# Kernel tuning notes

Hardware: AMD Instinct MI355X
Metric: run time of the kernel (lower is better)

## Reference

```python
import jax, jax.numpy as jnp
import numpy as np

N = 100000  # nodes
E = 1600000  # edges
F = 128      # nfeat == nclass (source constructs every layer as nfeat->nclass)


def setup_inputs() -> dict:
    key = jax.random.key(0)
    ks = jax.random.split(key, 8)
    x = jax.random.normal(ks[0], (N, F), dtype=jnp.float32)
    row = jax.random.randint(ks[1], (E,), 0, N)
    col = jax.random.randint(ks[2], (E,), 0, N)
    s = (1.0 / np.sqrt(F)).astype(np.float32) if hasattr(1.0/np.sqrt(F), 'astype') else 1.0/np.sqrt(F)
    s = 1.0 / np.sqrt(F)
    W0 = jax.random.uniform(ks[3], (F, F), jnp.float32, -s, s)
    b0 = jax.random.uniform(ks[4], (F,), jnp.float32, -s, s)
    W1 = jax.random.uniform(ks[5], (F, F), jnp.float32, -s, s)
    b1 = jax.random.uniform(ks[6], (F,), jnp.float32, -s, s)
    return {"x": x, "W0": W0, "b0": b0, "W1": W1, "b1": b1, "row": row, "col": col}


def _gcn_layer(h_in, W, b, row, col, dinv):
    # h = Linear(feat)
    h = h_in @ W + b
    # (D^-1/2 (A+I) D^-1/2) @ h, A in COO (row=i, col=j), A[i,j]=1
    coef = dinv[row] * dinv[col]                      # [E]
    msg = h[col] * coef[:, None]                       # [E, F] gather
    agg = jax.ops.segment_sum(msg, row, num_segments=N)
    agg = agg + (dinv * dinv)[:, None] * h             # self loops (identity)
    return agg


def reference(x, W0, b0, W1, b1, row, col):
    # D_hat = diag((A + I).sum(0)) -> column sums + 1
    deg = jax.ops.segment_sum(jnp.ones((E,), jnp.float32), col, num_segments=N) + 1.0
    dinv = deg ** -0.5
    h = _gcn_layer(x, W0, b0, row, col, dinv)
    h = jax.nn.relu(h)            # with_relu=True; dropout off (eval mode)
    h = _gcn_layer(h, W1, b1, row, col, dinv)
    return jax.nn.log_softmax(h, axis=1)
```

## Files before the change

### kernel.cpp

```cpp
#include <hip/hip_runtime.h>
#include <math.h>

#define FDIM 128
#define RPB 256
#define BSTRIDE 32
#define NBLK 512
#define MAXB 512
#define NSUB 8
#define SCAP 1024
#define CAP (NSUB * SCAP)

typedef __attribute__((ext_vector_type(8))) short short8;
typedef __attribute__((ext_vector_type(4))) float floatx4;

static __device__ __forceinline__ unsigned short f2bf(float f) {
    unsigned int u = __float_as_uint(f);
    u = (u + 0x7fff + ((u >> 16) & 1)) >> 16;
    return (unsigned short)u;
}

static __device__ __forceinline__ unsigned int cvtpk(float a, float b) {
    unsigned int r;
    asm("v_cvt_pk_bf16_f32 %0, %1, %2" : "=v"(r) : "v"(a), "v"(b));
    return r;
}

static __device__ __forceinline__ void bf2f(unsigned int u, float& a, float& b) {
    a = __uint_as_float(u << 16);
    b = __uint_as_float(u & 0xffff0000u);
}


__global__ __launch_bounds__(256) void k_init(int* rbCnt, int* cbCnt, int nb, unsigned int* hsz,
                                              const float* __restrict__ W0, const float* __restrict__ W1,
                                              unsigned short* __restrict__ W0t, unsigned short* __restrict__ W1t) {
    const int b = blockIdx.x;
    const int tid = threadIdx.x;
    if (b >= 2) {
        int i0 = (b - 2) * 256 + tid;
        int tot = nb * NSUB;
        for (int i = i0; i < tot; i += (gridDim.x - 2) * 256) {
            rbCnt[(size_t)i * BSTRIDE] = 0;
            cbCnt[(size_t)i * BSTRIDE] = 0;
        }
        if (b == 2 && tid < 64) hsz[tid] = 0u;
    } else {
        const float* W = (b == 0) ? W0 : W1;
        unsigned short* Wt = (b == 0) ? W0t : W1t;
        for (int idx = tid; idx < FDIM * FDIM; idx += 256) {
            int k = idx >> 7, c = idx & 127;
            Wt[c * FDIM + k] = f2bf(W[idx]);
        }
    }
}


__global__ __launch_bounds__(256) void k_scatter(const int* __restrict__ row, const int* __restrict__ col,
                                                 int* rbCnt, int* cbCnt,
                                                 unsigned int* __restrict__ pairs,
                                                 unsigned char* __restrict__ clocal, int nE, int nb) {
    __shared__ int rh[MAXB];
    __shared__ int ch[MAXB];
    __shared__ int rbase[MAXB];
    __shared__ int cbase[MAXB];
    const int tid = threadIdx.x;
    const int sub = blockIdx.x & (NSUB - 1);
    const int cpb = (nE + NBLK - 1) / NBLK;
    const int e0 = blockIdx.x * cpb;
    int e1 = e0 + cpb; if (e1 > nE) e1 = nE;

    for (int i = tid; i < nb; i += 256) { rh[i] = 0; ch[i] = 0; }
    __syncthreads();
    for (int e = e0 + tid; e < e1; e += 256) {
        atomicAdd(&rh[row[e] >> 8], 1);
        atomicAdd(&ch[col[e] >> 8], 1);
    }
    __syncthreads();
    for (int i = tid; i < nb; i += 256) {
        rbase[i] = rh[i] ? (i * CAP + sub * SCAP +
                            atomicAdd(&rbCnt[(size_t)(i * NSUB + sub) * BSTRIDE], rh[i])) : 0;
        cbase[i] = ch[i] ? (i * CAP + sub * SCAP +
                            atomicAdd(&cbCnt[(size_t)(i * NSUB + sub) * BSTRIDE], ch[i])) : 0;
        rh[i] = 0;
        ch[i] = 0;
    }
    __syncthreads();
    const int pmax = nb * CAP - 1;
    for (int e = e0 + tid; e < e1; e += 256) {
        int r = row[e];
        int c = col[e];
        int rb = r >> 8, cb = c >> 8;
        int p = rbase[rb] + atomicAdd(&rh[rb], 1);
        if (p > pmax) p = pmax;
        pairs[p] = ((unsigned int)(r & (RPB - 1)) << 24) | (unsigned int)c;
        int q = cbase[cb] + atomicAdd(&ch[cb], 1);
        if (q > pmax) q = pmax;
        clocal[q] = (unsigned char)(c & (RPB - 1));
    }
}


__global__ __launch_bounds__(256) void k_sortdinv(const int* __restrict__ rbCnt, const int* __restrict__ cbCnt,
                                                  const unsigned int* __restrict__ pairs,
                                                  const unsigned char* __restrict__ clocal,
                                                  uint2* __restrict__ rse, float* __restrict__ dinv,
                                                  int* __restrict__ csr_col, int n, int nb) {
    __shared__ int chist[RPB];
    __shared__ int hist[RPB];
    __shared__ int scan[RPB];
    __shared__ int lcur[RPB];
    const int b = blockIdx.x;
    const int tid = threadIdx.x;
    const int row0 = b * RPB;

    hist[tid] = 0;
    chist[tid] = 0;
    __syncthreads();
#pragma unroll
    for (int s = 0; s < NSUB; s++) {
        int rc = rbCnt[(size_t)(b * NSUB + s) * BSTRIDE]; if (rc > SCAP) rc = SCAP;
        int cc = cbCnt[(size_t)(b * NSUB + s) * BSTRIDE]; if (cc > SCAP) cc = SCAP;
        const int seg0 = b * CAP + s * SCAP;
        for (int i = seg0 + tid; i < seg0 + rc; i += 256)
            atomicAdd(&hist[pairs[i] >> 24], 1);
        for (int i = seg0 + tid; i < seg0 + cc; i += 256)
            atomicAdd(&chist[(int)clocal[i]], 1);
    }
    __syncthreads();

    scan[tid] = hist[tid];
    __syncthreads();
    for (int off = 1; off < RPB; off <<= 1) {
        int t = (tid >= off) ? scan[tid - off] : 0;
        __syncthreads();
        scan[tid] += t;
        __syncthreads();
    }
    {
        int ex = b * CAP + scan[tid] - hist[tid];
        lcur[tid] = ex;
        int r = row0 + tid;
        if (r < n) {
            rse[r] = make_uint2((unsigned int)ex, (unsigned int)(ex + hist[tid]));
            dinv[r] = rsqrtf((float)chist[tid] + 1.0f);
        }
    }
    __syncthreads();

#pragma unroll
    for (int s = 0; s < NSUB; s++) {
        int rc = rbCnt[(size_t)(b * NSUB + s) * BSTRIDE]; if (rc > SCAP) rc = SCAP;
        const int seg0 = b * CAP + s * SCAP;
        for (int i = seg0 + tid; i < seg0 + rc; i += 256) {
            unsigned int u = pairs[i];
            int pos = atomicAdd(&lcur[u >> 24], 1);
            csr_col[pos] = (int)(u & 0x00FFFFFFu);
        }
    }
}


#define KH 64
#define LPAD 72

__global__ __launch_bounds__(256) void k_gemm_mfma(const void* __restrict__ Ain,
                                                   const unsigned short* __restrict__ Wt,
                                                   const float* __restrict__ bias,
                                                   const float* __restrict__ dinv,
                                                   unsigned int* __restrict__ outp, int n, int af32) {
    __shared__ unsigned short sA[128][LPAD];
    __shared__ unsigned short sW[128][LPAD];

    const unsigned short* A = (const unsigned short*)Ain;
    const float* Af = (const float*)Ain;

    const int tid = threadIdx.x;
    const int row0 = blockIdx.x * 128;
    const int wid = tid >> 6;
    const int lane = tid & 63;
    const int quad = lane >> 4;
    const int lq = lane & 15;
    const int wm = wid & 1;
    const int wn = wid >> 1;

    floatx4 acc[4][4];
#pragma unroll
    for (int i = 0; i < 4; i++)
#pragma unroll
        for (int j = 0; j < 4; j++) acc[i][j] = (floatx4){0.f, 0.f, 0.f, 0.f};

    for (int kh = 0; kh < 2; kh++) {
        if (kh) __syncthreads();
#pragma unroll
        for (int it = 0; it < 4; it++) {
            int f = tid + it * 256;
            int r = f >> 3;
            int c8 = (f & 7) * 8;
            int gr = row0 + r;
            if (af32) {
                float4 v0 = make_float4(0.f, 0.f, 0.f, 0.f);
                float4 v1 = make_float4(0.f, 0.f, 0.f, 0.f);
                if (gr < n) {
                    v0 = *(const float4*)&Af[(size_t)gr * FDIM + kh * KH + c8];
                    v1 = *(const float4*)&Af[(size_t)gr * FDIM + kh * KH + c8 + 4];
                }
                uint4 p;
                p.x = cvtpk(v0.x, v0.y);
                p.y = cvtpk(v0.z, v0.w);
                p.z = cvtpk(v1.x, v1.y);
                p.w = cvtpk(v1.z, v1.w);
                *(uint4*)&sA[r][c8] = p;
            } else {
                uint4 v = make_uint4(0u, 0u, 0u, 0u);
                if (gr < n) v = *(const uint4*)&A[(size_t)gr * FDIM + kh * KH + c8];
                *(uint4*)&sA[r][c8] = v;
            }
            uint4 wv = *(const uint4*)&Wt[(size_t)r * FDIM + kh * KH + c8];
            *(uint4*)&sW[r][c8] = wv;
        }
        __syncthreads();

#pragma unroll
        for (int kt = 0; kt < 2; kt++) {
            const int k0 = kt * 32 + quad * 8;
            short8 af[4], bf[4];
#pragma unroll
            for (int mt = 0; mt < 4; mt++)
                af[mt] = *(const short8*)&sA[wm * 64 + mt * 16 + lq][k0];
#pragma unroll
            for (int nt = 0; nt < 4; nt++)
                bf[nt] = *(const short8*)&sW[wn * 64 + nt * 16 + lq][k0];
#pragma unroll
            for (int mt = 0; mt < 4; mt++)
#pragma unroll
                for (int nt = 0; nt < 4; nt++)
                    acc[mt][nt] = __builtin_amdgcn_mfma_f32_16x16x32_bf16(af[mt], bf[nt], acc[mt][nt], 0, 0, 0);
        }
    }

    float bv[4];
#pragma unroll
    for (int nt = 0; nt < 4; nt++) bv[nt] = bias[wn * 64 + nt * 16 + lq];

#pragma unroll
    for (int mt = 0; mt < 4; mt++) {
#pragma unroll
        for (int r = 0; r < 4; r++) {
            int grow = row0 + wm * 64 + mt * 16 + quad * 4 + r;
            float di = (grow < n) ? dinv[grow] : 0.f;
#pragma unroll
            for (int nt = 0; nt < 4; nt++) {
                float v = (acc[mt][nt][r] + bv[nt]) * di;
                float pv = __shfl_xor(v, 1, 64);
                if (!(lq & 1) && grow < n) {
                    int col = wn * 64 + nt * 16 + lq;
                    outp[(size_t)grow * 64 + (col >> 1)] =
                        (unsigned int)f2bf(v) | ((unsigned int)f2bf(pv) << 16);
                }
            }
        }
    }
}


#define UACC(U) { float p_, q_; \
    bf2f(U.x, p_, q_); acc0 += p_; acc1 += q_; \
    bf2f(U.y, p_, q_); acc2 += p_; acc3 += q_; \
    bf2f(U.z, p_, q_); acc4 += p_; acc5 += q_; \
    bf2f(U.w, p_, q_); acc6 += p_; acc7 += q_; }

__global__ __launch_bounds__(256) void k_agg(const unsigned int* __restrict__ hs,
                                             const uint2* __restrict__ rse,
                                             const int* __restrict__ csr_col, const float* __restrict__ dinv,
                                             void* __restrict__ out, int n, int relu, int lsm, int obf) {
    int w = (blockIdx.x * 256 + threadIdx.x) >> 6;
    int lane = threadIdx.x & 63;
    if (w >= n) return;
    const int quad = lane >> 4;
    const int lq = lane & 15;

    const uint2 se = rse[w];
    int e = (int)se.x;
    const int end = (int)se.y;
    const float di = dinv[w];

    uint4 sv = make_uint4(0u, 0u, 0u, 0u);
    if (quad == 0) sv = *(const uint4*)&hs[(size_t)w * 64 + lq * 4];
    float acc0, acc1, acc2, acc3, acc4, acc5, acc6, acc7;
    bf2f(sv.x, acc0, acc1);
    bf2f(sv.y, acc2, acc3);
    bf2f(sv.z, acc4, acc5);
    bf2f(sv.w, acc6, acc7);

    const int zrow = n;

    while (e < end) {
        int cnt = end - e;
        if (cnt > 64) cnt = 64;
        int jv = (e + lane < end) ? csr_col[e + lane] : zrow;
        int nb8 = (cnt + 7) >> 3;
        for (int t = 0; t < nb8; t++) {
            int i0 = t * 8 + quad;
            int j0 = __shfl(jv, i0, 64);
            int j1 = __shfl(jv, i0 + 4, 64);
            uint4 u0 = *(const uint4*)&hs[(size_t)j0 * 64 + lq * 4];
            uint4 u1 = *(const uint4*)&hs[(size_t)j1 * 64 + lq * 4];
            UACC(u0)
            UACC(u1)
        }
        e += cnt;
    }

    acc0 += __shfl_xor(acc0, 16, 64); acc0 += __shfl_xor(acc0, 32, 64);
    acc1 += __shfl_xor(acc1, 16, 64); acc1 += __shfl_xor(acc1, 32, 64);
    acc2 += __shfl_xor(acc2, 16, 64); acc2 += __shfl_xor(acc2, 32, 64);
    acc3 += __shfl_xor(acc3, 16, 64); acc3 += __shfl_xor(acc3, 32, 64);
    acc4 += __shfl_xor(acc4, 16, 64); acc4 += __shfl_xor(acc4, 32, 64);
    acc5 += __shfl_xor(acc5, 16, 64); acc5 += __shfl_xor(acc5, 32, 64);
    acc6 += __shfl_xor(acc6, 16, 64); acc6 += __shfl_xor(acc6, 32, 64);
    acc7 += __shfl_xor(acc7, 16, 64); acc7 += __shfl_xor(acc7, 32, 64);

    acc0 *= di; acc1 *= di; acc2 *= di; acc3 *= di;
    acc4 *= di; acc5 *= di; acc6 *= di; acc7 *= di;
    if (relu) {
        acc0 = fmaxf(acc0, 0.f); acc1 = fmaxf(acc1, 0.f);
        acc2 = fmaxf(acc2, 0.f); acc3 = fmaxf(acc3, 0.f);
        acc4 = fmaxf(acc4, 0.f); acc5 = fmaxf(acc5, 0.f);
        acc6 = fmaxf(acc6, 0.f); acc7 = fmaxf(acc7, 0.f);
    }
    if (lsm) {
        float m = fmaxf(fmaxf(fmaxf(acc0, acc1), fmaxf(acc2, acc3)),
                        fmaxf(fmaxf(acc4, acc5), fmaxf(acc6, acc7)));
#pragma unroll
        for (int off = 1; off < 16; off <<= 1) m = fmaxf(m, __shfl_xor(m, off, 64));
        float s = ((expf(acc0 - m) + expf(acc1 - m)) + (expf(acc2 - m) + expf(acc3 - m))) +
                  ((expf(acc4 - m) + expf(acc5 - m)) + (expf(acc6 - m) + expf(acc7 - m)));
#pragma unroll
        for (int off = 1; off < 16; off <<= 1) s += __shfl_xor(s, off, 64);
        float lg = m + logf(s);
        acc0 -= lg; acc1 -= lg; acc2 -= lg; acc3 -= lg;
        acc4 -= lg; acc5 -= lg; acc6 -= lg; acc7 -= lg;
    }
    if (obf) {
        if (quad == 0) {
            uint4 o;
            o.x = (unsigned int)f2bf(acc0) | ((unsigned int)f2bf(acc1) << 16);
            o.y = (unsigned int)f2bf(acc2) | ((unsigned int)f2bf(acc3) << 16);
            o.z = (unsigned int)f2bf(acc4) | ((unsigned int)f2bf(acc5) << 16);
            o.w = (unsigned int)f2bf(acc6) | ((unsigned int)f2bf(acc7) << 16);
            *(uint4*)((unsigned int*)out + (size_t)w * 64 + lq * 4) = o;
        }
    } else {
        if (quad < 2) {
            float4 o = quad ? make_float4(acc4, acc5, acc6, acc7)
                            : make_float4(acc0, acc1, acc2, acc3);
            *(float4*)((float*)out + (size_t)w * 128 + lq * 8 + quad * 4) = o;
        }
    }
}


extern "C" void kernel_launch(void* const* d_in, const int* in_sizes, int n_in,
                              void* d_out, int out_size, void* d_ws, size_t ws_size,
                              hipStream_t stream) {
    const float* x  = (const float*)d_in[0];
    const float* W0 = (const float*)d_in[1];
    const float* b0 = (const float*)d_in[2];
    const float* W1 = (const float*)d_in[3];
    const float* b1 = (const float*)d_in[4];
    const int* row  = (const int*)d_in[5];
    const int* col  = (const int*)d_in[6];
    float* out = (float*)d_out;

    const int N = in_sizes[0] / FDIM;
    const int E = in_sizes[5];
    const int NB = (N + RPB - 1) / RPB;

    char* w = (char*)d_ws;
    size_t off = 0;
    auto alloc = [&](size_t bytes) {
        char* p = w + off;
        off += (bytes + 255) & ~(size_t)255;
        return p;
    };
    int* rbCnt   = (int*)alloc((size_t)NB * NSUB * BSTRIDE * 4);
    int* cbCnt   = (int*)alloc((size_t)NB * NSUB * BSTRIDE * 4);
    float* dinv  = (float*)alloc((size_t)N * 4);
    uint2* rse   = (uint2*)alloc((size_t)N * 8);
    int* csr_col = (int*)alloc((size_t)NB * CAP * 4);
    unsigned short* W0t = (unsigned short*)alloc((size_t)FDIM * FDIM * 2);
    unsigned short* W1t = (unsigned short*)alloc((size_t)FDIM * FDIM * 2);
    unsigned int* hs = (unsigned int*)alloc((size_t)(N + 1) * 64 * 4);
    size_t pairsSz = (size_t)NB * CAP * 4;
    size_t clocSz  = (size_t)NB * CAP;
    size_t uniSz   = pairsSz + clocSz + 512;
    size_t hbSz    = (size_t)N * 64 * 4;
    char* uni = (char*)alloc(uniSz > hbSz ? uniSz : hbSz);
    unsigned int* pairs = (unsigned int*)uni;
    unsigned char* clocal = (unsigned char*)(uni + pairsSz);
    unsigned int* hb = (unsigned int*)uni;

    const int gW = (N * 64 + 255) / 256;
    const int gG = (N + 127) / 128;

    k_init<<<18, 256, 0, stream>>>(rbCnt, cbCnt, NB, hs + (size_t)N * 64, W0, W1, W0t, W1t);
    k_scatter<<<NBLK, 256, 0, stream>>>(row, col, rbCnt, cbCnt, pairs, clocal, E, NB);
    k_sortdinv<<<NB, 256, 0, stream>>>(rbCnt, cbCnt, pairs, clocal, rse, dinv, csr_col, N, NB);

    k_gemm_mfma<<<gG, 256, 0, stream>>>((const void*)x, W0t, b0, dinv, hs, N, 1);
    k_agg<<<gW, 256, 0, stream>>>(hs, rse, csr_col, dinv, hb, N, 1, 0, 1);

    k_gemm_mfma<<<gG, 256, 0, stream>>>((const void*)hb, W1t, b1, dinv, hs, N, 0);
    k_agg<<<gW, 256, 0, stream>>>(hs, rse, csr_col, dinv, out, N, 0, 1, 0);
}
```

Measured before the change: 353.8 us.

## Fuse first-layer GEMM into scatter kernel and move dinv scaling into aggregation

```diff
diff --git a/kernel.cpp b/kernel.cpp
--- a/kernel.cpp
+++ b/kernel.cpp
@@ -32,6 +32,7 @@
 
 
 __global__ __launch_bounds__(256) void k_init(int* rbCnt, int* cbCnt, int nb, unsigned int* hsz,
+                                              float* dinvN,
                                               const float* __restrict__ W0, const float* __restrict__ W1,
                                               unsigned short* __restrict__ W0t, unsigned short* __restrict__ W1t) {
     const int b = blockIdx.x;
@@ -44,6 +45,7 @@
             cbCnt[(size_t)i * BSTRIDE] = 0;
         }
         if (b == 2 && tid < 64) hsz[tid] = 0u;
+        if (b == 2 && tid == 64) *dinvN = 0.0f;
     } else {
         const float* W = (b == 0) ? W0 : W1;
         unsigned short* Wt = (b == 0) ? W0t : W1t;
@@ -55,127 +57,24 @@
 }
 
 
-__global__ __launch_bounds__(256) void k_scatter(const int* __restrict__ row, const int* __restrict__ col,
-                                                 int* rbCnt, int* cbCnt,
-                                                 unsigned int* __restrict__ pairs,
-                                                 unsigned char* __restrict__ clocal, int nE, int nb) {
-    __shared__ int rh[MAXB];
-    __shared__ int ch[MAXB];
-    __shared__ int rbase[MAXB];
-    __shared__ int cbase[MAXB];
-    const int tid = threadIdx.x;
-    const int sub = blockIdx.x & (NSUB - 1);
-    const int cpb = (nE + NBLK - 1) / NBLK;
-    const int e0 = blockIdx.x * cpb;
-    int e1 = e0 + cpb; if (e1 > nE) e1 = nE;
-
-    for (int i = tid; i < nb; i += 256) { rh[i] = 0; ch[i] = 0; }
-    __syncthreads();
-    for (int e = e0 + tid; e < e1; e += 256) {
-        atomicAdd(&rh[row[e] >> 8], 1);
-        atomicAdd(&ch[col[e] >> 8], 1);
-    }
-    __syncthreads();
-    for (int i = tid; i < nb; i += 256) {
-        rbase[i] = rh[i] ? (i * CAP + sub * SCAP +
-                            atomicAdd(&rbCnt[(size_t)(i * NSUB + sub) * BSTRIDE], rh[i])) : 0;
-        cbase[i] = ch[i] ? (i * CAP + sub * SCAP +
-                            atomicAdd(&cbCnt[(size_t)(i * NSUB + sub) * BSTRIDE], ch[i])) : 0;
-        rh[i] = 0;
-        ch[i] = 0;
-    }
-    __syncthreads();
-    const int pmax = nb * CAP - 1;
-    for (int e = e0 + tid; e < e1; e += 256) {
-        int r = row[e];
-        int c = col[e];
-        int rb = r >> 8, cb = c >> 8;
-        int p = rbase[rb] + atomicAdd(&rh[rb], 1);
-        if (p > pmax) p = pmax;
-        pairs[p] = ((unsigned int)(r & (RPB - 1)) << 24) | (unsigned int)c;
-        int q = cbase[cb] + atomicAdd(&ch[cb], 1);
-        if (q > pmax) q = pmax;
-        clocal[q] = (unsigned char)(c & (RPB - 1));
-    }
-}
-
-
-__global__ __launch_bounds__(256) void k_sortdinv(const int* __restrict__ rbCnt, const int* __restrict__ cbCnt,
-                                                  const unsigned int* __restrict__ pairs,
-                                                  const unsigned char* __restrict__ clocal,
-                                                  uint2* __restrict__ rse, float* __restrict__ dinv,
-                                                  int* __restrict__ csr_col, int n, int nb) {
-    __shared__ int chist[RPB];
-    __shared__ int hist[RPB];
-    __shared__ int scan[RPB];
-    __shared__ int lcur[RPB];
-    const int b = blockIdx.x;
-    const int tid = threadIdx.x;
-    const int row0 = b * RPB;
-
-    hist[tid] = 0;
-    chist[tid] = 0;
-    __syncthreads();
-#pragma unroll
-    for (int s = 0; s < NSUB; s++) {
-        int rc = rbCnt[(size_t)(b * NSUB + s) * BSTRIDE]; if (rc > SCAP) rc = SCAP;
-        int cc = cbCnt[(size_t)(b * NSUB + s) * BSTRIDE]; if (cc > SCAP) cc = SCAP;
-        const int seg0 = b * CAP + s * SCAP;
-        for (int i = seg0 + tid; i < seg0 + rc; i += 256)
-            atomicAdd(&hist[pairs[i] >> 24], 1);
-        for (int i = seg0 + tid; i < seg0 + cc; i += 256)
-            atomicAdd(&chist[(int)clocal[i]], 1);
-    }
-    __syncthreads();
-
-    scan[tid] = hist[tid];
-    __syncthreads();
-    for (int off = 1; off < RPB; off <<= 1) {
-        int t = (tid >= off) ? scan[tid - off] : 0;
-        __syncthreads();
-        scan[tid] += t;
-        __syncthreads();
-    }
-    {
-        int ex = b * CAP + scan[tid] - hist[tid];
-        lcur[tid] = ex;
-        int r = row0 + tid;
-        if (r < n) {
-            rse[r] = make_uint2((unsigned int)ex, (unsigned int)(ex + hist[tid]));
-            dinv[r] = rsqrtf((float)chist[tid] + 1.0f);
-        }
-    }
-    __syncthreads();
-
-#pragma unroll
-    for (int s = 0; s < NSUB; s++) {
-        int rc = rbCnt[(size_t)(b * NSUB + s) * BSTRIDE]; if (rc > SCAP) rc = SCAP;
-        const int seg0 = b * CAP + s * SCAP;
-        for (int i = seg0 + tid; i < seg0 + rc; i += 256) {
-            unsigned int u = pairs[i];
-            int pos = atomicAdd(&lcur[u >> 24], 1);
-            csr_col[pos] = (int)(u & 0x00FFFFFFu);
-        }
-    }
-}
-
-
 #define KH 64
 #define LPAD 72
-
-__global__ __launch_bounds__(256) void k_gemm_mfma(const void* __restrict__ Ain,
-                                                   const unsigned short* __restrict__ Wt,
-                                                   const float* __restrict__ bias,
-                                                   const float* __restrict__ dinv,
-                                                   unsigned int* __restrict__ outp, int n, int af32) {
-    __shared__ unsigned short sA[128][LPAD];
-    __shared__ unsigned short sW[128][LPAD];
+#define GSMEM (2 * 128 * LPAD * 2)
+
+static __device__ __forceinline__ void gemm_body(char* smem, const void* __restrict__ Ain,
+                                                 const unsigned short* __restrict__ Wt,
+                                                 const float* __restrict__ bias,
+                                                 const float* __restrict__ dinv,
+                                                 unsigned int* __restrict__ outp, int n,
+                                                 int af32, int scaled, int blk) {
+    unsigned short (*sA)[LPAD] = (unsigned short(*)[LPAD])smem;
+    unsigned short (*sW)[LPAD] = (unsigned short(*)[LPAD])(smem + 128 * LPAD * 2);
 
     const unsigned short* A = (const unsigned short*)Ain;
     const float* Af = (const float*)Ain;
 
     const int tid = threadIdx.x;
-    const int row0 = blockIdx.x * 128;
+    const int row0 = blk * 128;
     const int wid = tid >> 6;
     const int lane = tid & 63;
     const int quad = lane >> 4;
@@ -247,7 +146,7 @@
 #pragma unroll
         for (int r = 0; r < 4; r++) {
             int grow = row0 + wm * 64 + mt * 16 + quad * 4 + r;
-            float di = (grow < n) ? dinv[grow] : 0.f;
+            float di = scaled ? ((grow < n) ? dinv[grow] : 0.f) : 1.0f;
 #pragma unroll
             for (int nt = 0; nt < 4; nt++) {
                 float v = (acc[mt][nt][r] + bv[nt]) * di;
@@ -263,16 +162,148 @@
 }
 
 
+__global__ __launch_bounds__(256) void k_scatter_gemm(const int* __restrict__ row, const int* __restrict__ col,
+                                                      int* rbCnt, int* cbCnt,
+                                                      unsigned int* __restrict__ pairs,
+                                                      unsigned char* __restrict__ clocal, int nE, int nb,
+                                                      const float* __restrict__ x,
+                                                      const unsigned short* __restrict__ W0t,
+                                                      const float* __restrict__ b0,
+                                                      unsigned int* __restrict__ hs, int n) {
+    __shared__ __align__(16) char smem[GSMEM];
+
+    if (blockIdx.x >= NBLK) {
+        gemm_body(smem, (const void*)x, W0t, b0, (const float*)nullptr, hs, n, 1, 0, blockIdx.x - NBLK);
+        return;
+    }
+
+    int* rh    = (int*)smem;
+    int* ch    = (int*)(smem + MAXB * 4);
+    int* rbase = (int*)(smem + MAXB * 8);
+    int* cbase = (int*)(smem + MAXB * 12);
+    const int tid = threadIdx.x;
+    const int sub = blockIdx.x & (NSUB - 1);
+    const int cpb = (nE + NBLK - 1) / NBLK;
+    const int e0 = blockIdx.x * cpb;
+    int e1 = e0 + cpb; if (e1 > nE) e1 = nE;
+
+    for (int i = tid; i < nb; i += 256) { rh[i] = 0; ch[i] = 0; }
+    __syncthreads();
+    for (int e = e0 + tid; e < e1; e += 256) {
+        atomicAdd(&rh[row[e] >> 8], 1);
+        atomicAdd(&ch[col[e] >> 8], 1);
+    }
+    __syncthreads();
+    for (int i = tid; i < nb; i += 256) {
+        rbase[i] = rh[i] ? (i * CAP + sub * SCAP +
+                            atomicAdd(&rbCnt[(size_t)(i * NSUB + sub) * BSTRIDE], rh[i])) : 0;
+        cbase[i] = ch[i] ? (i * CAP + sub * SCAP +
+                            atomicAdd(&cbCnt[(size_t)(i * NSUB + sub) * BSTRIDE], ch[i])) : 0;
+        rh[i] = 0;
+        ch[i] = 0;
+    }
+    __syncthreads();
+    const int pmax = nb * CAP - 1;
+    for (int e = e0 + tid; e < e1; e += 256) {
+        int r = row[e];
+        int c = col[e];
+        int rb = r >> 8, cb = c >> 8;
+        int p = rbase[rb] + atomicAdd(&rh[rb], 1);
+        if (p > pmax) p = pmax;
+        pairs[p] = ((unsigned int)(r & (RPB - 1)) << 24) | (unsigned int)c;
+        int q = cbase[cb] + atomicAdd(&ch[cb], 1);
+        if (q > pmax) q = pmax;
+        clocal[q] = (unsigned char)(c & (RPB - 1));
+    }
+}
+
+
+__global__ __launch_bounds__(256) void k_sortdinv(const int* __restrict__ rbCnt, const int* __restrict__ cbCnt,
+                                                  const unsigned int* __restrict__ pairs,
+                                                  const unsigned char* __restrict__ clocal,
+                                                  uint2* __restrict__ rse, float* __restrict__ dinv,
+                                                  int* __restrict__ csr_col, int n, int nb) {
+    __shared__ int chist[RPB];
+    __shared__ int hist[RPB];
+    __shared__ int scan[RPB];
+    __shared__ int lcur[RPB];
+    const int b = blockIdx.x;
+    const int tid = threadIdx.x;
+    const int row0 = b * RPB;
+
+    hist[tid] = 0;
+    chist[tid] = 0;
+    __syncthreads();
+#pragma unroll
+    for (int s = 0; s < NSUB; s++) {
+        int rc = rbCnt[(size_t)(b * NSUB + s) * BSTRIDE]; if (rc > SCAP) rc = SCAP;
+        int cc = cbCnt[(size_t)(b * NSUB + s) * BSTRIDE]; if (cc > SCAP) cc = SCAP;
+        const int seg0 = b * CAP + s * SCAP;
+        for (int i = seg0 + tid; i < seg0 + rc; i += 256)
+            atomicAdd(&hist[pairs[i] >> 24], 1);
+        for (int i = seg0 + tid; i < seg0 + cc; i += 256)
+            atomicAdd(&chist[(int)clocal[i]], 1);
+    }
+    __syncthreads();
+
+    scan[tid] = hist[tid];
+    __syncthreads();
+    for (int off = 1; off < RPB; off <<= 1) {
+        int t = (tid >= off) ? scan[tid - off] : 0;
+        __syncthreads();
+        scan[tid] += t;
+        __syncthreads();
+    }
+    {
+        int ex = b * CAP + scan[tid] - hist[tid];
+        lcur[tid] = ex;
+        int r = row0 + tid;
+        if (r < n) {
+            rse[r] = make_uint2((unsigned int)ex, (unsigned int)(ex + hist[tid]));
+            dinv[r] = rsqrtf((float)chist[tid] + 1.0f);
+        }
+    }
+    __syncthreads();
+
+#pragma unroll
+    for (int s = 0; s < NSUB; s++) {
+        int rc = rbCnt[(size_t)(b * NSUB + s) * BSTRIDE]; if (rc > SCAP) rc = SCAP;
+        const int seg0 = b * CAP + s * SCAP;
+        for (int i = seg0 + tid; i < seg0 + rc; i += 256) {
+            unsigned int u = pairs[i];
+            int pos = atomicAdd(&lcur[u >> 24], 1);
+            csr_col[pos] = (int)(u & 0x00FFFFFFu);
+        }
+    }
+}
+
+
+__global__ __launch_bounds__(256) void k_gemm_mfma(const void* __restrict__ Ain,
+                                                   const unsigned short* __restrict__ Wt,
+                                                   const float* __restrict__ bias,
+                                                   const float* __restrict__ dinv,
+                                                   unsigned int* __restrict__ outp, int n, int af32) {
+    __shared__ __align__(16) char smem[GSMEM];
+    gemm_body(smem, Ain, Wt, bias, dinv, outp, n, af32, 1, blockIdx.x);
+}
+
+
 #define UACC(U) { float p_, q_; \
     bf2f(U.x, p_, q_); acc0 += p_; acc1 += q_; \
     bf2f(U.y, p_, q_); acc2 += p_; acc3 += q_; \
     bf2f(U.z, p_, q_); acc4 += p_; acc5 += q_; \
     bf2f(U.w, p_, q_); acc6 += p_; acc7 += q_; }
 
+#define UACCD(U, DJ) { float p_, q_; \
+    bf2f(U.x, p_, q_); acc0 = fmaf(p_, DJ, acc0); acc1 = fmaf(q_, DJ, acc1); \
+    bf2f(U.y, p_, q_); acc2 = fmaf(p_, DJ, acc2); acc3 = fmaf(q_, DJ, acc3); \
+    bf2f(U.z, p_, q_); acc4 = fmaf(p_, DJ, acc4); acc5 = fmaf(q_, DJ, acc5); \
+    bf2f(U.w, p_, q_); acc6 = fmaf(p_, DJ, acc6); acc7 = fmaf(q_, DJ, acc7); }
+
 __global__ __launch_bounds__(256) void k_agg(const unsigned int* __restrict__ hs,
                                              const uint2* __restrict__ rse,
                                              const int* __restrict__ csr_col, const float* __restrict__ dinv,
-                                             void* __restrict__ out, int n, int relu, int lsm, int obf) {
+                                             void* __restrict__ out, int n, int relu, int lsm, int obf, int es) {
     int w = (blockIdx.x * 256 + threadIdx.x) >> 6;
     int lane = threadIdx.x & 63;
     if (w >= n) return;
@@ -291,6 +322,10 @@
     bf2f(sv.y, acc2, acc3);
     bf2f(sv.z, acc4, acc5);
     bf2f(sv.w, acc6, acc7);
+    if (es) {
+        acc0 *= di; acc1 *= di; acc2 *= di; acc3 *= di;
+        acc4 *= di; acc5 *= di; acc6 *= di; acc7 *= di;
+    }
 
     const int zrow = n;
 
@@ -305,8 +340,15 @@
             int j1 = __shfl(jv, i0 + 4, 64);
             uint4 u0 = *(const uint4*)&hs[(size_t)j0 * 64 + lq * 4];
             uint4 u1 = *(const uint4*)&hs[(size_t)j1 * 64 + lq * 4];
-            UACC(u0)
-            UACC(u1)
+            if (es) {
+                float dj0 = dinv[j0];
+                float dj1 = dinv[j1];
+                UACCD(u0, dj0)
+                UACCD(u1, dj1)
+            } else {
+                UACC(u0)
+                UACC(u1)
+            }
         }
         e += cnt;
     }
@@ -385,7 +427,7 @@
     };
     int* rbCnt   = (int*)alloc((size_t)NB * NSUB * BSTRIDE * 4);
     int* cbCnt   = (int*)alloc((size_t)NB * NSUB * BSTRIDE * 4);
-    float* dinv  = (float*)alloc((size_t)N * 4);
+    float* dinv  = (float*)alloc((size_t)(N + 1) * 4);
     uint2* rse   = (uint2*)alloc((size_t)N * 8);
     int* csr_col = (int*)alloc((size_t)NB * CAP * 4);
     unsigned short* W0t = (unsigned short*)alloc((size_t)FDIM * FDIM * 2);
@@ -403,13 +445,13 @@
     const int gW = (N * 64 + 255) / 256;
     const int gG = (N + 127) / 128;
 
-    k_init<<<18, 256, 0, stream>>>(rbCnt, cbCnt, NB, hs + (size_t)N * 64, W0, W1, W0t, W1t);
-    k_scatter<<<NBLK, 256, 0, stream>>>(row, col, rbCnt, cbCnt, pairs, clocal, E, NB);
+    k_init<<<16, 256, 0, stream>>>(rbCnt, cbCnt, NB, hs + (size_t)N * 64, dinv + N, W0, W1, W0t, W1t);
+    k_scatter_gemm<<<NBLK + gG, 256, 0, stream>>>(row, col, rbCnt, cbCnt, pairs, clocal, E, NB,
+                                                  x, W0t, b0, hs, N);
     k_sortdinv<<<NB, 256, 0, stream>>>(rbCnt, cbCnt, pairs, clocal, rse, dinv, csr_col, N, NB);
 
-    k_gemm_mfma<<<gG, 256, 0, stream>>>((const void*)x, W0t, b0, dinv, hs, N, 1);
-    k_agg<<<gW, 256, 0, stream>>>(hs, rse, csr_col, dinv, hb, N, 1, 0, 1);
+    k_agg<<<gW, 256, 0, stream>>>(hs, rse, csr_col, dinv, hb, N, 1, 0, 1, 1);
 
     k_gemm_mfma<<<gG, 256, 0, stream>>>((const void*)hb, W1t, b1, dinv, hs, N, 0);
-    k_agg<<<gW, 256, 0, stream>>>(hs, rse, csr_col, dinv, out, N, 0, 1, 0);
-}
+    k_agg<<<gW, 256, 0, stream>>>(hs, rse, csr_col, dinv, out, N, 0, 1, 0, 0);
+}
```

After: 346.8 us. -2.0%, faster.
